# Performance work log

Hardware: AMD Instinct MI355X
Metric: run time of the kernel (lower is better)

The kernel has to match this reference:

```python
import jax, jax.numpy as jnp
import numpy as np

MIN_NORM = 1e-15
BALL_EPS = 1e-3   # project() margin from ball boundary (c = 1)
TANH_CLIP = 15.0


def _norm(x):
    return jnp.sqrt(jnp.sum(x * x, axis=-1, keepdims=True)).clip(MIN_NORM)


def _tanh(x):
    return jnp.tanh(jnp.clip(x, -TANH_CLIP, TANH_CLIP))


def _artanh(x):
    return jnp.arctanh(jnp.clip(x, -1.0 + 1e-7, 1.0 - 1e-7))


def mobius_add(x, y):
    # Poincare ball Mobius addition, curvature c = 1
    x2 = jnp.sum(x * x, axis=-1, keepdims=True)
    y2 = jnp.sum(y * y, axis=-1, keepdims=True)
    xy = jnp.sum(x * y, axis=-1, keepdims=True)
    num = (1.0 + 2.0 * xy + y2) * x + (1.0 - x2) * y
    den = 1.0 + 2.0 * xy + x2 * y2
    return num / den.clip(MIN_NORM)


def project(x):
    norm = _norm(x)
    maxnorm = 1.0 - BALL_EPS
    return jnp.where(norm > maxnorm, x * (maxnorm / norm), x)


def expmap0(u):
    # exp map at the origin
    n = _norm(u)
    return _tanh(n) * u / n


def expmap(u, p):
    # exp map of tangent vector u at base point p
    n = _norm(u)
    p2 = jnp.sum(p * p, axis=-1, keepdims=True)
    lam = 2.0 / (1.0 - p2).clip(MIN_NORM)
    second = _tanh(0.5 * lam * n) * u / n
    return mobius_add(p, second)


def logmap(y, x):
    # log map of point y at base point x
    sub = mobius_add(-x, y)
    n = _norm(sub)
    x2 = jnp.sum(x * x, axis=-1, keepdims=True)
    lam = 2.0 / (1.0 - x2).clip(MIN_NORM)
    return (2.0 / lam) * _artanh(n) * sub / n


def setup_inputs() -> dict:
    key = jax.random.key(0)
    k1, k2, k3, k4 = jax.random.split(key, 4)
    n_entities, n_edges, n_rel, d = 100000, 800000, 32, 64
    # scale embeddings down so points stay well inside the unit ball
    ego_embed = 0.1 * jax.random.normal(k1, (n_entities, d), dtype=jnp.float32)
    relation_embed = 0.1 * jax.random.normal(k2, (n_rel, d), dtype=jnp.float32)
    edge_index = jax.random.randint(k3, (2, n_edges), 0, n_entities, dtype=jnp.int64)
    edge_type = jax.random.randint(k4, (n_edges,), 0, n_rel, dtype=jnp.int64)
    return {"ego_embed": ego_embed, "edge_index": edge_index,
            "edge_type": edge_type, "relation_embed": relation_embed}


def reference(ego_embed, edge_index, edge_type, relation_embed):
    head, tail = edge_index[0], edge_index[1]
    n_entities = ego_embed.shape[0]
    head_emb = ego_embed[head]          # [E, d] gather
    tail_emb = ego_embed[tail]          # [E, d] gather
    relation_emb = relation_embed[edge_type]  # [E, d] gather
    hyper_head = expmap0(head_emb)
    hyper_tail = expmap(tail_emb, hyper_head)
    hyper_rel = expmap(relation_emb, hyper_head)
    res = project(mobius_add(hyper_tail, hyper_rel))
    res = logmap(res, hyper_head)
    # scatter_mean over head index
    sums = jax.ops.segment_sum(res, head, num_segments=n_entities)
    counts = jax.ops.segment_sum(jnp.ones((head.shape[0],), dtype=res.dtype),
                                 head, num_segments=n_entities)
    entity_agg = sums / jnp.maximum(counts, 1.0)[:, None]
    return entity_agg
```

## Files before the change

### kernel.cpp

```cpp
#include <hip/hip_runtime.h>
#include <math.h>

#define D 64
#define MAXNORM 0.999f
#define MAXNORM2 (0.999f * 0.999f)
#define MIN_NORM 1e-15f
#define TANH_CLIP 15.0f
#define CHUNK 1024

struct f4 { float x, y, z, w; };

__device__ __forceinline__ float frcp(float x) { return __builtin_amdgcn_rcpf(x); }
__device__ __forceinline__ float frsq(float x) { return __builtin_amdgcn_rsqf(x); }

__device__ __forceinline__ float dot8p(const f4& a0, const f4& a1,
                                       const f4& b0, const f4& b1) {
    return a0.x * b0.x + a0.y * b0.y + a0.z * b0.z + a0.w * b0.w +
           a1.x * b1.x + a1.y * b1.y + a1.z * b1.z + a1.w * b1.w;
}

__device__ __forceinline__ float rsum8(float v) {
    v += __shfl_xor(v, 1);
    v += __shfl_xor(v, 2);
    v += __shfl_xor(v, 4);
    return v;
}


__global__ void hist_kernel(const int* __restrict__ eidx,
                            int* __restrict__ cnt,
                            int* __restrict__ rank, int E) {
    int e = blockIdx.x * blockDim.x + threadIdx.x;
    if (e < E) rank[e] = atomicAdd(&cnt[eidx[e]], 1);
}


__global__ void scan_kernel(const int* __restrict__ cnt,
                            int* __restrict__ off,
                            const float* __restrict__ ego,
                            const float* __restrict__ rel,
                            float* __restrict__ norms,
                            float* __restrict__ relnorm,
                            float2* __restrict__ scal,
                            int N, int NB, int E) {
    if (blockIdx.x >= NB) {
        int wid = (blockIdx.x - NB) * 4 + (threadIdx.x >> 6);
        int lane = threadIdx.x & 63;
        if (wid >= N + 32) return;
        const float* src = (wid < N) ? (ego + (size_t)wid * D)
                                     : (rel + (size_t)(wid - N) * D);
        float v = src[lane];
        float s = v * v;
        s += __shfl_xor(s, 1);  s += __shfl_xor(s, 2);  s += __shfl_xor(s, 4);
        s += __shfl_xor(s, 8);  s += __shfl_xor(s, 16); s += __shfl_xor(s, 32);
        if (lane == 0) {
            float nh = sqrtf(s);
            if (wid < N) {
                norms[wid] = nh;
                float nhc = fmaxf(nh, MIN_NORM);
                float eh  = __expf(-2.0f * fminf(nhc, TANH_CLIP));
                float fp  = (1.0f - eh) * frcp((1.0f + eh) * nhc);
                float th2 = fp * fp * nhc * nhc;
                float tol = fmaxf(1.0f - th2, MIN_NORM);
                scal[wid] = make_float2(fp, tol);
            } else {
                relnorm[wid - N] = nh;
            }
        }
        return;
    }

    __shared__ int sdata[256];
    __shared__ int sprefix;
    int tid = threadIdx.x;
    int base0 = blockIdx.x * CHUNK;

    if (blockIdx.x == 0 && tid == 0) off[N] = E;

    int psum = 0;
    const int4* cnt4 = (const int4*)cnt;
    for (int i = tid; i < (base0 >> 2); i += 256) {
        int4 v = cnt4[i];
        psum += v.x + v.y + v.z + v.w;
    }
    sdata[tid] = psum;
    __syncthreads();
    for (int o = 128; o > 0; o >>= 1) {
        if (tid < o) sdata[tid] += sdata[tid + o];
        __syncthreads();
    }
    if (tid == 0) sprefix = sdata[0];
    __syncthreads();
    int prefix = sprefix;
    __syncthreads();

    int base = base0 + tid * 4;
    int v0 = (base + 0 < N) ? cnt[base + 0] : 0;
    int v1 = (base + 1 < N) ? cnt[base + 1] : 0;
    int v2 = (base + 2 < N) ? cnt[base + 2] : 0;
    int v3 = (base + 3 < N) ? cnt[base + 3] : 0;
    sdata[tid] = v0 + v1 + v2 + v3;
    __syncthreads();
    for (int o = 1; o < 256; o <<= 1) {
        int add = (tid >= o) ? sdata[tid - o] : 0;
        __syncthreads();
        sdata[tid] += add;
        __syncthreads();
    }
    int run = prefix + ((tid > 0) ? sdata[tid - 1] : 0);
    if (base + 0 < N) { off[base + 0] = run; run += v0; }
    if (base + 1 < N) { off[base + 1] = run; run += v1; }
    if (base + 2 < N) { off[base + 2] = run; run += v2; }
    if (base + 3 < N) { off[base + 3] = run; run += v3; }
}


__global__ void scatter_kernel(const int* __restrict__ eidx,
                               const int* __restrict__ etype,
                               const int* __restrict__ rank,
                               const int* __restrict__ off,
                               const float* __restrict__ norms,
                               const float2* __restrict__ scal,
                               float4* __restrict__ payA, int E) {
    int e = blockIdx.x * blockDim.x + threadIdx.x;
    if (e >= E) return;
    int head = eidx[e];
    int tail = eidx[E + e];
    int type = etype[e];
    int pos  = off[head] + rank[e];

    float2 sc2 = scal[head];
    float fp  = sc2.x;
    float tol = sc2.y;
    float hl  = frcp(tol);
    float nt  = norms[tail];
    float ntc = fmaxf(nt, MIN_NORM);
    float et  = __expf(-2.0f * fminf(hl * ntc, TANH_CLIP));
    float ft  = (1.0f - et) * frcp((1.0f + et) * ntc);
    float gt  = ft * nt;

    payA[pos] = make_float4(__int_as_float(tail | (type << 17)),
                            fp * ft, gt * gt, tol * ft);
}


__global__ void __launch_bounds__(256) agg_kernel(
        const float* __restrict__ ego,
        const float* __restrict__ rel,
        const int* __restrict__ off,
        const float4* __restrict__ payA,
        const float* __restrict__ relnorm,
        const float2* __restrict__ scal,
        float* __restrict__ out,
        int N) {
    int wid = (blockIdx.x * blockDim.x + threadIdx.x) >> 6;
    if (wid >= N) return;
    int lane = threadIdx.x & 63;
    int slot = lane >> 3;
    int sub  = lane & 7;

    int h = wid;
    const float* hrow = ego + (size_t)h * D;
    f4 h0 = *(const f4*)(hrow + sub * 4);
    f4 h1 = *(const f4*)(hrow + 32 + sub * 4);

    float2 sc2 = scal[h];
    float fp  = sc2.x;
    float tol = sc2.y;
    float p2  = 1.0f - tol;
    float hl  = frcp(tol);

    int o = off[h];
    int c = off[h + 1] - o;
    f4 a0 = {0.f, 0.f, 0.f, 0.f}, a1 = {0.f, 0.f, 0.f, 0.f};
    float accP = 0.f;

    for (int i = slot; i < c; i += 8) {
        float4 pa = payA[o + i];
        int pk   = __float_as_int(pa.x);
        int tail = pk & 0x1FFFF;
        int type = pk >> 17;

        const float* trow = ego + (size_t)tail * D;
        f4 t0 = *(const f4*)(trow + sub * 4);
        f4 t1 = *(const f4*)(trow + 32 + sub * 4);
        const float* rrow = rel + (size_t)type * D;
        f4 r0 = *(const f4*)(rrow + sub * 4);
        f4 r1 = *(const f4*)(rrow + 32 + sub * 4);
        float nr = relnorm[type];

        float d_ht = rsum8(dot8p(h0, h1, t0, t1));
        float d_hr = rsum8(dot8p(h0, h1, r0, r1));
        float d_tr = rsum8(dot8p(t0, t1, r0, r1));

        float pt = fp * d_ht;
        float pr = fp * d_hr;

        float pyt = pa.y * d_ht;
        float yt2 = pa.z;
        float o1t = fmaf(2.0f, pyt, 1.0f);
        float at  = o1t + yt2;
        float invt = frcp(fmaf(p2, yt2, o1t));
        float At = at * invt;
        float Bt = pa.w * invt;
        float x2 = (at - tol) * invt;

        float nrc = fmaxf(nr, MIN_NORM);
        float er  = __expf(-2.0f * fminf(hl * nrc, TANH_CLIP));
        float fr  = (1.0f - er) * frcp((1.0f + er) * nrc);
        float pyr = fr * pr;
        float gr  = fr * nr;
        float yr2 = gr * gr;
        float o1r = fmaf(2.0f, pyr, 1.0f);
        float ar  = o1r + yr2;
        float invr = frcp(fmaf(p2, yr2, o1r));
        float Ar = ar * invr;
        float Br = tol * fr * invr;
        float y2 = (ar - tol) * invr;

        float xy = At * Ar * p2 + At * Br * pr + Ar * Bt * pt + Bt * Br * d_tr;
        float o1m = fmaf(2.0f, xy, 1.0f);
        float am = o1m + y2;
        float bm = 1.0f - x2;
        float invm = frcp(fmaf(x2, y2, o1m));
        float al = (am * At + bm * Ar) * invm;
        float be = am * Bt * invm;
        float ga = bm * Br * invm;
        float m2 = fmaxf((am - bm) * invm, 1e-30f);

        if (m2 > MAXNORM2) {
            float s_ = MAXNORM * frsq(m2);
            al *= s_; be *= s_; ga *= s_;
            m2 = MAXNORM2;
        }

        float pm   = al * p2 + be * pt + ga * pr;
        float o2   = fmaf(-2.0f, pm, 1.0f);
        float invs = frcp(fmaf(p2, m2, o2));
        float om   = o2 + m2;
        float smm  = tol * invs;
        float u = fmaf(smm, al, -om * invs);
        float v = smm * be;
        float w = smm * ga;
        float s2 = fmaxf((om - tol) * invs, 1e-30f);

        float irs = frsq(s2);
        float ns  = fminf(s2 * irs, 1.0f - 1e-7f);
        float art = 0.5f * __logf((1.0f + ns) * frcp(1.0f - ns));
        float scv = tol * art * irs;

        float ct = scv * v, cr = scv * w;
        accP = fmaf(scv, u, accP);
        a0.x += ct * t0.x + cr * r0.x;  a0.y += ct * t0.y + cr * r0.y;
        a0.z += ct * t0.z + cr * r0.z;  a0.w += ct * t0.w + cr * r0.w;
        a1.x += ct * t1.x + cr * r1.x;  a1.y += ct * t1.y + cr * r1.y;
        a1.z += ct * t1.z + cr * r1.z;  a1.w += ct * t1.w + cr * r1.w;
    }

    #define RED(x) x += __shfl_xor(x, 8); x += __shfl_xor(x, 16); x += __shfl_xor(x, 32);
    RED(accP)
    RED(a0.x) RED(a0.y) RED(a0.z) RED(a0.w)
    RED(a1.x) RED(a1.y) RED(a1.z) RED(a1.w)
    #undef RED

    if (slot == 0) {
        float invc = frcp(fmaxf((float)c, 1.0f));
        float hp = accP * fp * invc;
        f4 o0, o1;
        o0.x = hp * h0.x + a0.x * invc;  o0.y = hp * h0.y + a0.y * invc;
        o0.z = hp * h0.z + a0.z * invc;  o0.w = hp * h0.w + a0.w * invc;
        o1.x = hp * h1.x + a1.x * invc;  o1.y = hp * h1.y + a1.y * invc;
        o1.z = hp * h1.z + a1.z * invc;  o1.w = hp * h1.w + a1.w * invc;
        float* orow = out + (size_t)h * D;
        *(f4*)(orow + sub * 4)      = o0;
        *(f4*)(orow + 32 + sub * 4) = o1;
    }
}

extern "C" void kernel_launch(void* const* d_in, const int* in_sizes, int n_in,
                              void* d_out, int out_size, void* d_ws, size_t ws_size,
                              hipStream_t stream) {
    const float* ego  = (const float*)d_in[0];
    const int*   eidx = (const int*)d_in[1];
    const int*   etyp = (const int*)d_in[2];
    const float* rel  = (const float*)d_in[3];
    float* out = (float*)d_out;

    int E = in_sizes[1] / 2;
    int N = in_sizes[0] / D;
    int NB = (N + CHUNK - 1) / CHUNK;

    float4* payA  = (float4*)d_ws;
    float2* scal  = (float2*)(payA + E);
    int* cnt      = (int*)(scal + N);
    int* off      = cnt + N;
    int* rank     = off + N + 1;
    float* norms   = (float*)(rank + E);
    float* relnorm = norms + N;

    hipMemsetAsync(cnt, 0, (size_t)N * sizeof(int), stream);

    const int tpb = 256;
    int eblocks = (E + tpb - 1) / tpb;
    int norm_blocks = (N + 32 + 3) / 4;

    hist_kernel<<<eblocks, tpb, 0, stream>>>(eidx, cnt, rank, E);
    scan_kernel<<<NB + norm_blocks, tpb, 0, stream>>>(cnt, off, ego, rel,
                                                      norms, relnorm, scal,
                                                      N, NB, E);
    scatter_kernel<<<eblocks, tpb, 0, stream>>>(eidx, etyp, rank, off,
                                                norms, scal, payA, E);

    int nblocks = (N + 3) / 4;
    agg_kernel<<<nblocks, tpb, 0, stream>>>(ego, rel, off, payA,
                                            relnorm, scal, out, N);
}
```

Baseline: 170.3 us.

## Precompute entity-relation dot table and move relation-side math to scatter

```diff
diff --git a/kernel.cpp b/kernel.cpp
--- a/kernel.cpp
+++ b/kernel.cpp
@@ -42,7 +42,23 @@
                             float* __restrict__ norms,
                             float* __restrict__ relnorm,
                             float2* __restrict__ scal,
-                            int N, int NB, int E) {
+                            float* __restrict__ HT,
+                            int N, int NB, int norm_blocks, int E) {
+    if (blockIdx.x >= NB + norm_blocks) {
+        int i = (blockIdx.x - NB - norm_blocks) * 256 + threadIdx.x;
+        if (i >= N * 32) return;
+        int n = i >> 5, k = i & 31;
+        const f4* hr = (const f4*)(ego + (size_t)n * D);
+        const f4* rr = (const f4*)(rel + (size_t)k * D);
+        float s = 0.f;
+        #pragma unroll
+        for (int j = 0; j < 16; j++) {
+            f4 a = hr[j], b = rr[j];
+            s += a.x * b.x + a.y * b.y + a.z * b.z + a.w * b.w;
+        }
+        HT[i] = s;
+        return;
+    }
     if (blockIdx.x >= NB) {
         int wid = (blockIdx.x - NB) * 4 + (threadIdx.x >> 6);
         int lane = threadIdx.x & 63;
@@ -120,8 +136,11 @@
                                const int* __restrict__ rank,
                                const int* __restrict__ off,
                                const float* __restrict__ norms,
+                               const float* __restrict__ relnorm,
                                const float2* __restrict__ scal,
-                               float4* __restrict__ payA, int E) {
+                               const float* __restrict__ HT,
+                               float4* __restrict__ payA,
+                               float4* __restrict__ payB, int E) {
     int e = blockIdx.x * blockDim.x + threadIdx.x;
     if (e >= E) return;
     int head = eidx[e];
@@ -132,15 +151,34 @@
     float2 sc2 = scal[head];
     float fp  = sc2.x;
     float tol = sc2.y;
+    float p2  = 1.0f - tol;
     float hl  = frcp(tol);
+
     float nt  = norms[tail];
     float ntc = fmaxf(nt, MIN_NORM);
     float et  = __expf(-2.0f * fminf(hl * ntc, TANH_CLIP));
     float ft  = (1.0f - et) * frcp((1.0f + et) * ntc);
     float gt  = ft * nt;
 
+    float nr  = relnorm[type];
+    float nrc = fmaxf(nr, MIN_NORM);
+    float er  = __expf(-2.0f * fminf(hl * nrc, TANH_CLIP));
+    float fr  = (1.0f - er) * frcp((1.0f + er) * nrc);
+    float d_hr = HT[head * 32 + type];
+    float pyr = fr * fp * d_hr;
+    float gr  = fr * nr;
+    float yr2 = gr * gr;
+    float o1r = fmaf(2.0f, pyr, 1.0f);
+    float ar  = o1r + yr2;
+    float invr = frcp(fmaf(p2, yr2, o1r));
+    float Ar = ar * invr;
+    float Br = tol * fr * invr;
+    float y2 = (ar - tol) * invr;
+    float d_tr = HT[tail * 32 + type];
+
     payA[pos] = make_float4(__int_as_float(tail | (type << 17)),
                             fp * ft, gt * gt, tol * ft);
+    payB[pos] = make_float4(Ar, Br, y2, d_tr);
 }
 
 
@@ -149,7 +187,8 @@
         const float* __restrict__ rel,
         const int* __restrict__ off,
         const float4* __restrict__ payA,
-        const float* __restrict__ relnorm,
+        const float4* __restrict__ payB,
+        const float* __restrict__ HT,
         const float2* __restrict__ scal,
         float* __restrict__ out,
         int N) {
@@ -168,7 +207,7 @@
     float fp  = sc2.x;
     float tol = sc2.y;
     float p2  = 1.0f - tol;
-    float hl  = frcp(tol);
+    const float* htrow = HT + (size_t)h * 32;
 
     int o = off[h];
     int c = off[h + 1] - o;
@@ -177,6 +216,7 @@
 
     for (int i = slot; i < c; i += 8) {
         float4 pa = payA[o + i];
+        float4 pb = payB[o + i];
         int pk   = __float_as_int(pa.x);
         int tail = pk & 0x1FFFF;
         int type = pk >> 17;
@@ -187,12 +227,9 @@
         const float* rrow = rel + (size_t)type * D;
         f4 r0 = *(const f4*)(rrow + sub * 4);
         f4 r1 = *(const f4*)(rrow + 32 + sub * 4);
-        float nr = relnorm[type];
+        float d_hr = htrow[type];
 
         float d_ht = rsum8(dot8p(h0, h1, t0, t1));
-        float d_hr = rsum8(dot8p(h0, h1, r0, r1));
-        float d_tr = rsum8(dot8p(t0, t1, r0, r1));
-
         float pt = fp * d_ht;
         float pr = fp * d_hr;
 
@@ -205,18 +242,7 @@
         float Bt = pa.w * invt;
         float x2 = (at - tol) * invt;
 
-        float nrc = fmaxf(nr, MIN_NORM);
-        float er  = __expf(-2.0f * fminf(hl * nrc, TANH_CLIP));
-        float fr  = (1.0f - er) * frcp((1.0f + er) * nrc);
-        float pyr = fr * pr;
-        float gr  = fr * nr;
-        float yr2 = gr * gr;
-        float o1r = fmaf(2.0f, pyr, 1.0f);
-        float ar  = o1r + yr2;
-        float invr = frcp(fmaf(p2, yr2, o1r));
-        float Ar = ar * invr;
-        float Br = tol * fr * invr;
-        float y2 = (ar - tol) * invr;
+        float Ar = pb.x, Br = pb.y, y2 = pb.z, d_tr = pb.w;
 
         float xy = At * Ar * p2 + At * Br * pr + Ar * Bt * pt + Bt * Br * d_tr;
         float o1m = fmaf(2.0f, xy, 1.0f);
@@ -291,7 +317,9 @@
     int NB = (N + CHUNK - 1) / CHUNK;
 
     float4* payA  = (float4*)d_ws;
-    float2* scal  = (float2*)(payA + E);
+    float4* payB  = payA + E;
+    float*  HT    = (float*)(payB + E);
+    float2* scal  = (float2*)(HT + (size_t)N * 32);
     int* cnt      = (int*)(scal + N);
     int* off      = cnt + N;
     int* rank     = off + N + 1;
@@ -303,15 +331,16 @@
     const int tpb = 256;
     int eblocks = (E + tpb - 1) / tpb;
     int norm_blocks = (N + 32 + 3) / 4;
+    int ht_blocks = (N * 32 + tpb - 1) / tpb;
 
     hist_kernel<<<eblocks, tpb, 0, stream>>>(eidx, cnt, rank, E);
-    scan_kernel<<<NB + norm_blocks, tpb, 0, stream>>>(cnt, off, ego, rel,
-                                                      norms, relnorm, scal,
-                                                      N, NB, E);
+    scan_kernel<<<NB + norm_blocks + ht_blocks, tpb, 0, stream>>>(
+        cnt, off, ego, rel, norms, relnorm, scal, HT, N, NB, norm_blocks, E);
     scatter_kernel<<<eblocks, tpb, 0, stream>>>(eidx, etyp, rank, off,
-                                                norms, scal, payA, E);
+                                                norms, relnorm, scal, HT,
+                                                payA, payB, E);
 
     int nblocks = (N + 3) / 4;
-    agg_kernel<<<nblocks, tpb, 0, stream>>>(ego, rel, off, payA,
-                                            relnorm, scal, out, N);
-}
+    agg_kernel<<<nblocks, tpb, 0, stream>>>(ego, rel, off, payA, payB,
+                                            HT, scal, out, N);
+}
```

Measured after the change: 297.6 us. 74.7% more time.
